# Optimization experiments

Hardware: AMD Instinct MI355X
Metric: run time of the kernel (lower is better)

The kernel has to match this reference:

```python
import jax, jax.numpy as jnp
import numpy as np

B, S, E = 2, 2048, 2048
A, H = 2048, 16  # attention_dim, n_heads
HD = A // H      # head_dim = 128
ROPE_THETA = 10000.0


def setup_inputs() -> dict:
    key = jax.random.key(0)
    k1, k2, k3 = jax.random.split(key, 3)
    x = jax.random.normal(k1, (B, S, E), dtype=jnp.float32)
    W_qkv = jax.random.normal(k2, (E, 3 * A), dtype=jnp.float32) * 0.02
    W_out = jax.random.normal(k3, (A, E), dtype=jnp.float32) * 0.02
    return {"x": x, "W_qkv": W_qkv, "W_out": W_out}


def _apply_rope(x):
    # x: (B, H, S, D); interleaved rotary pairs (rotary-embedding-torch default)
    b, h, s, d = x.shape
    inv_freq = 1.0 / (ROPE_THETA ** (jnp.arange(0, d, 2, dtype=jnp.float32) / d))
    freqs = jnp.arange(s, dtype=jnp.float32)[:, None] * inv_freq[None, :]  # (S, D/2)
    cos, sin = jnp.cos(freqs), jnp.sin(freqs)
    xr = x.reshape(b, h, s, d // 2, 2)
    x1, x2 = xr[..., 0], xr[..., 1]
    o1 = x1 * cos - x2 * sin
    o2 = x1 * sin + x2 * cos
    return jnp.stack([o1, o2], axis=-1).reshape(b, h, s, d)


def reference(x, W_qkv, W_out):
    b, s, _ = x.shape
    qkv = (x @ W_qkv).reshape(b, s, 3, H, HD)          # (B,S,3,H,hd)
    qkv = jnp.moveaxis(qkv, 3, 1)                      # movedim(-2,1) -> (B,H,S,3,hd)
    q, k, v = qkv[..., 0, :], qkv[..., 1, :], qkv[..., 2, :]
    q = _apply_rope(q)
    k = _apply_rope(k)
    scale = 1.0 / jnp.sqrt(jnp.asarray(HD, dtype=x.dtype))
    scores = jnp.einsum("bhqd,bhkd->bhqk", q, k) * scale
    attn = jax.nn.softmax(scores, axis=-1)
    out = jnp.einsum("bhqk,bhkd->bhqd", attn, v)       # (B,H,S,hd)
    out = out.transpose(0, 2, 1, 3).reshape(b, s, A)   # (B,S,A)
    return out @ W_out
```

## Files before the change

kernel.cpp:

```cpp
#include <hip/hip_runtime.h>
#include <math.h>

typedef float  f32x4 __attribute__((ext_vector_type(4)));
typedef short  s16x8 __attribute__((ext_vector_type(8)));
typedef short  s16x4 __attribute__((ext_vector_type(4)));
typedef unsigned short u16;
typedef unsigned int u32;

static __device__ __forceinline__ u16 f32_to_bf16_rne(float f) {
    u32 u = __builtin_bit_cast(u32, f);
    u32 r = u + 0x7fffu + ((u >> 16) & 1u);
    return (u16)(r >> 16);
}
static __device__ __forceinline__ u16 f32_to_bf16_rhu(float f) {
    u32 u = __builtin_bit_cast(u32, f);
    return (u16)((u + 0x8000u) >> 16);
}
static __device__ __forceinline__ float bf16_to_f32(u16 h) {
    return __builtin_bit_cast(float, (u32)h << 16);
}

static __device__ __forceinline__ void gl2lds16(const void* g, void* l) {
    __builtin_amdgcn_global_load_lds(
        (const __attribute__((address_space(1))) u32*)g,
        (__attribute__((address_space(3))) u32*)l, 16, 0, 0);
}

__global__ void k_cast(const float* __restrict__ in, u16* __restrict__ out) {
    int i = (blockIdx.x * 256 + threadIdx.x) * 4;
    float4 v = *reinterpret_cast<const float4*>(in + i);
    ushort4 u;
    u.x = f32_to_bf16_rne(v.x); u.y = f32_to_bf16_rne(v.y);
    u.z = f32_to_bf16_rne(v.z); u.w = f32_to_bf16_rne(v.w);
    *reinterpret_cast<ushort4*>(out + i) = u;
}

__global__ void k_transpose_cast(const float* __restrict__ in, u16* __restrict__ out,
                                 int R, int C) {
    __shared__ __align__(16) float tile[64 * 68];
    const int ct = blockIdx.x, rt = blockIdx.y;
    const int t = threadIdx.x;
    const int tr = t >> 4;
    const int tc4 = (t & 15) * 4;
#pragma unroll
    for (int rn = 0; rn < 4; ++rn) {
        int r = rn * 16 + tr;
        float4 v = *reinterpret_cast<const float4*>(in + (size_t)(rt * 64 + r) * C + ct * 64 + tc4);
        *reinterpret_cast<float4*>(&tile[r * 68 + tc4]) = v;
    }
    __syncthreads();
#pragma unroll
    for (int rn = 0; rn < 4; ++rn) {
        int oc = rn * 16 + tr;
        ushort4 u;
        u.x = f32_to_bf16_rne(tile[(tc4 + 0) * 68 + oc]);
        u.y = f32_to_bf16_rne(tile[(tc4 + 1) * 68 + oc]);
        u.z = f32_to_bf16_rne(tile[(tc4 + 2) * 68 + oc]);
        u.w = f32_to_bf16_rne(tile[(tc4 + 3) * 68 + oc]);
        *reinterpret_cast<ushort4*>(out + (size_t)(ct * 64 + oc) * R + rt * 64 + tc4) = u;
    }
}

template<bool BF16OUT, bool ROPE>
__global__ __launch_bounds__(256) void k_gemm_bt(const u16* __restrict__ Amat,
                                                 const u16* __restrict__ Bt,
                                                 void* __restrict__ Cout,
                                                 int M, int N, int K) {
    __shared__ __align__(16) u16 As[128 * 64];
    __shared__ __align__(16) u16 Bs[128 * 64];
    const int t = threadIdx.x;
    const int lane = t & 63, wave = t >> 6;
    const int m16 = lane & 15, qd = lane >> 4;
    const int wm = (wave >> 1) * 64, wn = (wave & 1) * 64;
    const size_t m0 = (size_t)blockIdx.y * 128, n0 = (size_t)blockIdx.x * 128;
    const int srow = lane >> 3;
    const int schunk = (lane & 7) ^ srow;

    f32x4 acc[4][4] = {};

    for (int k0 = 0; k0 < K; k0 += 64) {
#pragma unroll
        for (int j = 0; j < 4; ++j) {
            int rbase = j * 32 + wave * 8;
            int r = rbase + srow;
            gl2lds16(Amat + (m0 + r) * (size_t)K + k0 + schunk * 8, &As[rbase * 64]);
            gl2lds16(Bt   + (n0 + r) * (size_t)K + k0 + schunk * 8, &Bs[rbase * 64]);
        }
        __syncthreads();
#pragma unroll
        for (int kh = 0; kh < 2; ++kh) {
            s16x8 af[4], bf[4];
#pragma unroll
            for (int i = 0; i < 4; ++i) {
                int ra = wm + i * 16 + m16;
                int pa = (kh * 4 + qd) ^ (ra & 7);
                af[i] = *reinterpret_cast<const s16x8*>(&As[ra * 64 + pa * 8]);
                int rb = wn + i * 16 + m16;
                int pb = (kh * 4 + qd) ^ (rb & 7);
                bf[i] = *reinterpret_cast<const s16x8*>(&Bs[rb * 64 + pb * 8]);
            }
#pragma unroll
            for (int i = 0; i < 4; ++i)
#pragma unroll
                for (int jj = 0; jj < 4; ++jj)
                    acc[i][jj] = __builtin_amdgcn_mfma_f32_16x16x32_bf16(af[i], bf[jj], acc[i][jj], 0, 0, 0);
        }
        __syncthreads();
    }
    if (ROPE && n0 < 4096) {
        float invf[4];
#pragma unroll
        for (int j = 0; j < 4; ++j) {
            int pi = ((int)(wn + j * 16 + m16) & 127) >> 1;
            invf[j] = __expf(-0.14391156831f * (float)pi);
        }
#pragma unroll
        for (int i = 0; i < 4; ++i)
#pragma unroll
            for (int j = 0; j < 4; ++j)
#pragma unroll
                for (int r = 0; r < 4; ++r) {
                    float v = acc[i][j][r];
                    float p = __shfl_xor(v, 1);
                    size_t row = m0 + wm + i * 16 + qd * 4 + r;
                    float f = (float)(int)(row & 2047) * invf[j];
                    float sn, cs;
                    __sincosf(f, &sn, &cs);
                    float res = (m16 & 1) ? fmaf(p, sn, v * cs) : fmaf(v, cs, -p * sn);
                    size_t col = n0 + wn + j * 16 + m16;
                    ((u16*)Cout)[row * N + col] = f32_to_bf16_rne(res);
                }
    } else {
#pragma unroll
        for (int i = 0; i < 4; ++i)
#pragma unroll
            for (int j = 0; j < 4; ++j)
#pragma unroll
                for (int r = 0; r < 4; ++r) {
                    size_t row = m0 + wm + i * 16 + qd * 4 + r;
                    size_t col = n0 + wn + j * 16 + m16;
                    if (BF16OUT)
                        ((u16*)Cout)[row * N + col] = f32_to_bf16_rne(acc[i][j][r]);
                    else
                        ((float*)Cout)[row * N + col] = acc[i][j][r];
                }
    }
}

__global__ void k_transpose_v(const u16* __restrict__ qkv, u16* __restrict__ vt) {
    __shared__ u16 tile[64 * 68];
    const int st = blockIdx.x;
    const int bhd = blockIdx.y;
    const int bh = bhd >> 1, dt = bhd & 1;
    const u16* src = qkv + (size_t)(bh >> 4) * 2048 * 6144 + 4096 + (size_t)(bh & 15) * 128 + dt * 64;
    const int t = threadIdx.x, tr = t >> 4, tc4 = (t & 15) * 4;
#pragma unroll
    for (int rn = 0; rn < 4; ++rn) {
        int s = rn * 16 + tr;
        *reinterpret_cast<ushort4*>(&tile[s * 68 + tc4]) =
            *reinterpret_cast<const ushort4*>(src + (size_t)(st * 64 + s) * 6144 + tc4);
    }
    __syncthreads();
    u16* dst = vt + ((size_t)bh * 128 + dt * 64) * 2048 + st * 64;
#pragma unroll
    for (int rn = 0; rn < 4; ++rn) {
        int d = rn * 16 + tr;
        ushort4 u;
        u.x = tile[(tc4 + 0) * 68 + d];
        u.y = tile[(tc4 + 1) * 68 + d];
        u.z = tile[(tc4 + 2) * 68 + d];
        u.w = tile[(tc4 + 3) * 68 + d];
        *reinterpret_cast<ushort4*>(dst + (size_t)d * 2048 + tc4) = u;
    }
}

__global__ __launch_bounds__(256, 2) void k_flash(const u16* __restrict__ qkv,
                                                  const u16* __restrict__ vt,
                                                  u16* __restrict__ out) {
    __shared__ __align__(16) u16 KS[128 * 136];
    __shared__ __align__(16) u16 VS[128 * 136];
    const int t = threadIdx.x, lane = t & 63, wave = t >> 6;
    const int m16 = lane & 15, qd = lane >> 4;
    const int bh = blockIdx.y, b = bh >> 4, h = bh & 15;
    const int q0 = blockIdx.x * 128;
    const int wq = wave * 32;
    const u16* Qg = qkv + (size_t)b * 2048 * 6144 + (size_t)h * 128;
    const u16* Kg = Qg + 2048;
    const u16* Vtg = vt + (size_t)bh * 128 * 2048;
    const float C2 = 0.12751743f;

    s16x8 qf[2][4];
#pragma unroll
    for (int mi = 0; mi < 2; ++mi)
#pragma unroll
        for (int kc = 0; kc < 4; ++kc)
            qf[mi][kc] = *reinterpret_cast<const s16x8*>(
                Qg + (size_t)(q0 + wq + mi * 16 + m16) * 6144 + kc * 32 + qd * 8);

    f32x4 accO[2][8] = {};
    float mrow[2] = {-1e30f, -1e30f};
    float lrow[2] = {0.f, 0.f};

    const int strow = t >> 4;
    const int stc = (t & 15) * 8;

    for (int kt = 0; kt < 16; ++kt) {
        const int s0 = kt * 128;
        __syncthreads();
#pragma unroll
        for (int rd = 0; rd < 8; ++rd) {
            int row = rd * 16 + strow;
            *reinterpret_cast<s16x8*>(&KS[row * 136 + stc]) =
                *reinterpret_cast<const s16x8*>(Kg + (size_t)(s0 + row) * 6144 + stc);
            *reinterpret_cast<s16x8*>(&VS[row * 136 + stc]) =
                *reinterpret_cast<const s16x8*>(Vtg + (size_t)row * 2048 + s0 + stc);
        }
        __syncthreads();

        f32x4 accS[2][8] = {};
#pragma unroll
        for (int kc = 0; kc < 4; ++kc)
#pragma unroll
            for (int nj = 0; nj < 8; ++nj) {
                s16x8 kf = *reinterpret_cast<const s16x8*>(
                    &KS[(nj * 16 + m16) * 136 + (kc * 4 + qd) * 8]);
                accS[0][nj] = __builtin_amdgcn_mfma_f32_16x16x32_bf16(kf, qf[0][kc], accS[0][nj], 0, 0, 0);
                accS[1][nj] = __builtin_amdgcn_mfma_f32_16x16x32_bf16(kf, qf[1][kc], accS[1][nj], 0, 0, 0);
            }

        s16x4 pk[2][8];
        float aO[2][4];
#pragma unroll
        for (int mi = 0; mi < 2; ++mi) {
            float mx = accS[mi][0][0];
#pragma unroll
            for (int nj = 0; nj < 8; ++nj)
#pragma unroll
                for (int r = 0; r < 4; ++r) mx = fmaxf(mx, accS[mi][nj][r]);
            mx *= C2;
            mx = fmaxf(mx, __shfl_xor(mx, 16));
            mx = fmaxf(mx, __shfl_xor(mx, 32));
            float mn = fmaxf(mrow[mi], mx);
            float alpha = exp2f(mrow[mi] - mn);
            mrow[mi] = mn;
            float ls = 0.f;
#pragma unroll
            for (int nj = 0; nj < 8; ++nj) {
                float p0 = exp2f(accS[mi][nj][0] * C2 - mn);
                float p1 = exp2f(accS[mi][nj][1] * C2 - mn);
                float p2 = exp2f(accS[mi][nj][2] * C2 - mn);
                float p3 = exp2f(accS[mi][nj][3] * C2 - mn);
                ls += (p0 + p1) + (p2 + p3);
                s16x4 pv;
                pv[0] = (short)f32_to_bf16_rhu(p0);
                pv[1] = (short)f32_to_bf16_rhu(p1);
                pv[2] = (short)f32_to_bf16_rhu(p2);
                pv[3] = (short)f32_to_bf16_rhu(p3);
                pk[mi][nj] = pv;
            }
            ls += __shfl_xor(ls, 16);
            ls += __shfl_xor(ls, 32);
            lrow[mi] = lrow[mi] * alpha + ls;
#pragma unroll
            for (int r = 0; r < 4; ++r)
                aO[mi][r] = __shfl(alpha, qd * 4 + r);
#pragma unroll
            for (int dj = 0; dj < 8; ++dj)
#pragma unroll
                for (int r = 0; r < 4; ++r) accO[mi][dj][r] *= aO[mi][r];
        }

#pragma unroll
        for (int kb = 0; kb < 4; ++kb) {
            s16x8 af0 = __builtin_shufflevector(pk[0][2 * kb], pk[0][2 * kb + 1],
                                                0, 1, 2, 3, 4, 5, 6, 7);
            s16x8 af1 = __builtin_shufflevector(pk[1][2 * kb], pk[1][2 * kb + 1],
                                                0, 1, 2, 3, 4, 5, 6, 7);
#pragma unroll
            for (int dj = 0; dj < 8; ++dj) {
                const u16* vrow = &VS[(dj * 16 + m16) * 136 + kb * 32 + qd * 4];
                s16x4 lo = *reinterpret_cast<const s16x4*>(vrow);
                s16x4 hi = *reinterpret_cast<const s16x4*>(vrow + 16);
                s16x8 vf = __builtin_shufflevector(lo, hi, 0, 1, 2, 3, 4, 5, 6, 7);
                accO[0][dj] = __builtin_amdgcn_mfma_f32_16x16x32_bf16(af0, vf, accO[0][dj], 0, 0, 0);
                accO[1][dj] = __builtin_amdgcn_mfma_f32_16x16x32_bf16(af1, vf, accO[1][dj], 0, 0, 0);
            }
        }
    }
#pragma unroll
    for (int mi = 0; mi < 2; ++mi) {
        float invl = 1.0f / lrow[mi];
        float iv[4];
#pragma unroll
        for (int r = 0; r < 4; ++r) iv[r] = __shfl(invl, qd * 4 + r);
#pragma unroll
        for (int r = 0; r < 4; ++r) {
            size_t row = (size_t)b * 2048 + q0 + wq + mi * 16 + qd * 4 + r;
#pragma unroll
            for (int dj = 0; dj < 8; ++dj)
                out[row * 2048 + h * 128 + dj * 16 + m16] =
                    f32_to_bf16_rne(accO[mi][dj][r] * iv[r]);
        }
    }
}

extern "C" void kernel_launch(void* const* d_in, const int* in_sizes, int n_in,
                              void* d_out, int out_size, void* d_ws, size_t ws_size,
                              hipStream_t stream) {
    const float* x     = (const float*)d_in[0];
    const float* W_qkv = (const float*)d_in[1];
    const float* W_out = (const float*)d_in[2];
    float* out = (float*)d_out;

    char* ws = (char*)d_ws;
    u16* xb   = (u16*)(ws);
    u16* Wqt  = (u16*)(ws + (16u << 20));
    u16* Wot  = (u16*)(ws + (40u << 20));
    u16* qkvb = (u16*)(ws + (48u << 20));
    u16* attn = (u16*)(ws + (96u << 20));
    u16* vtg  = (u16*)(ws + (112u << 20));

    k_cast<<<8192, 256, 0, stream>>>(x, xb);
    k_transpose_cast<<<dim3(96, 32), 256, 0, stream>>>(W_qkv, Wqt, 2048, 6144);
    k_transpose_cast<<<dim3(32, 32), 256, 0, stream>>>(W_out, Wot, 2048, 2048);
    k_gemm_bt<true, true><<<dim3(48, 32), 256, 0, stream>>>(xb, Wqt, qkvb, 4096, 6144, 2048);
    k_transpose_v<<<dim3(32, 64), 256, 0, stream>>>(qkvb, vtg);
    k_flash<<<dim3(16, 32), 256, 0, stream>>>(qkvb, vtg, attn);
    k_gemm_bt<false, false><<<dim3(16, 32), 256, 0, stream>>>(attn, Wot, out, 4096, 2048, 2048);
}
```

Baseline: 455.1 us.

## Restructure flash kernel to 8 waves of 16 query rows with register-staged loads

The flash attention block moves from 4 waves handling 32 query rows each to 8 waves handling 16 rows each. This halves per-wave register state so more waves can be resident and hide latency. K/V tile loads are now issued into registers before the barrier and then stored to LDS. V is stored in a permuted column order so each PV fragment is read with a single 16-byte LDS load. The softmax path also switches to the hardware exp2 intrinsic, fused multiply-add and paired bf16 packing. The cost is that each K/V tile in LDS is now shared by fewer query rows per wave, and the larger block adds barrier overhead.

After: 411.7 us. 1.11x faster.

```diff
diff --git a/kernel.cpp b/kernel.cpp
--- a/kernel.cpp
+++ b/kernel.cpp
@@ -12,9 +12,10 @@
     u32 r = u + 0x7fffu + ((u >> 16) & 1u);
     return (u16)(r >> 16);
 }
-static __device__ __forceinline__ u16 f32_to_bf16_rhu(float f) {
-    u32 u = __builtin_bit_cast(u32, f);
-    return (u16)((u + 0x8000u) >> 16);
+static __device__ __forceinline__ u32 pack_bf16_rhu(float a, float b) {
+    u32 ua = __builtin_bit_cast(u32, a);
+    u32 ub = __builtin_bit_cast(u32, b);
+    return ((ua + 0x8000u) >> 16) | ((ub + 0x8000u) & 0xffff0000u);
 }
 static __device__ __forceinline__ float bf16_to_f32(u16 h) {
     return __builtin_bit_cast(float, (u32)h << 16);
@@ -174,7 +175,7 @@
     }
 }
 
-__global__ __launch_bounds__(256, 2) void k_flash(const u16* __restrict__ qkv,
+__global__ __launch_bounds__(512, 4) void k_flash(const u16* __restrict__ qkv,
                                                   const u16* __restrict__ vt,
                                                   u16* __restrict__ out) {
     __shared__ __align__(16) u16 KS[128 * 136];
@@ -183,124 +184,120 @@
     const int m16 = lane & 15, qd = lane >> 4;
     const int bh = blockIdx.y, b = bh >> 4, h = bh & 15;
     const int q0 = blockIdx.x * 128;
-    const int wq = wave * 32;
     const u16* Qg = qkv + (size_t)b * 2048 * 6144 + (size_t)h * 128;
     const u16* Kg = Qg + 2048;
     const u16* Vtg = vt + (size_t)bh * 128 * 2048;
     const float C2 = 0.12751743f;
 
-    s16x8 qf[2][4];
-#pragma unroll
-    for (int mi = 0; mi < 2; ++mi)
-#pragma unroll
-        for (int kc = 0; kc < 4; ++kc)
-            qf[mi][kc] = *reinterpret_cast<const s16x8*>(
-                Qg + (size_t)(q0 + wq + mi * 16 + m16) * 6144 + kc * 32 + qd * 8);
-
-    f32x4 accO[2][8] = {};
-    float mrow[2] = {-1e30f, -1e30f};
-    float lrow[2] = {0.f, 0.f};
-
-    const int strow = t >> 4;
-    const int stc = (t & 15) * 8;
+    int srow[4], scol[4], pi0[4];
+#pragma unroll
+    for (int ci = 0; ci < 4; ++ci) {
+        int idx = ci * 512 + t;
+        int row = idx >> 4, c = idx & 15;
+        srow[ci] = row;
+        scol[ci] = c * 8;
+        pi0[ci] = 32 * (c >> 2) + 16 * (c & 1) + 4 * ((c >> 1) & 1);
+    }
+
+    s16x8 qf[4];
+#pragma unroll
+    for (int kc = 0; kc < 4; ++kc)
+        qf[kc] = *reinterpret_cast<const s16x8*>(
+            Qg + (size_t)(q0 + wave * 16 + m16) * 6144 + kc * 32 + qd * 8);
+
+    f32x4 accO[8] = {};
+    float mrow = -1e30f, lrow = 0.f;
 
     for (int kt = 0; kt < 16; ++kt) {
         const int s0 = kt * 128;
+        s16x8 kreg[4], vreg[4];
+#pragma unroll
+        for (int ci = 0; ci < 4; ++ci) {
+            kreg[ci] = *reinterpret_cast<const s16x8*>(
+                Kg + (size_t)(s0 + srow[ci]) * 6144 + scol[ci]);
+            vreg[ci] = *reinterpret_cast<const s16x8*>(
+                Vtg + (size_t)srow[ci] * 2048 + s0 + scol[ci]);
+        }
         __syncthreads();
 #pragma unroll
-        for (int rd = 0; rd < 8; ++rd) {
-            int row = rd * 16 + strow;
-            *reinterpret_cast<s16x8*>(&KS[row * 136 + stc]) =
-                *reinterpret_cast<const s16x8*>(Kg + (size_t)(s0 + row) * 6144 + stc);
-            *reinterpret_cast<s16x8*>(&VS[row * 136 + stc]) =
-                *reinterpret_cast<const s16x8*>(Vtg + (size_t)row * 2048 + s0 + stc);
+        for (int ci = 0; ci < 4; ++ci) {
+            *reinterpret_cast<s16x8*>(&KS[srow[ci] * 136 + scol[ci]]) = kreg[ci];
+            s16x4 lo = __builtin_shufflevector(vreg[ci], vreg[ci], 0, 1, 2, 3);
+            s16x4 hi = __builtin_shufflevector(vreg[ci], vreg[ci], 4, 5, 6, 7);
+            *reinterpret_cast<s16x4*>(&VS[srow[ci] * 136 + pi0[ci]]) = lo;
+            *reinterpret_cast<s16x4*>(&VS[srow[ci] * 136 + pi0[ci] + 8]) = hi;
         }
         __syncthreads();
 
-        f32x4 accS[2][8] = {};
+        f32x4 accS[8] = {};
 #pragma unroll
         for (int kc = 0; kc < 4; ++kc)
 #pragma unroll
             for (int nj = 0; nj < 8; ++nj) {
                 s16x8 kf = *reinterpret_cast<const s16x8*>(
                     &KS[(nj * 16 + m16) * 136 + (kc * 4 + qd) * 8]);
-                accS[0][nj] = __builtin_amdgcn_mfma_f32_16x16x32_bf16(kf, qf[0][kc], accS[0][nj], 0, 0, 0);
-                accS[1][nj] = __builtin_amdgcn_mfma_f32_16x16x32_bf16(kf, qf[1][kc], accS[1][nj], 0, 0, 0);
+                accS[nj] = __builtin_amdgcn_mfma_f32_16x16x32_bf16(kf, qf[kc], accS[nj], 0, 0, 0);
             }
 
-        s16x4 pk[2][8];
-        float aO[2][4];
-#pragma unroll
-        for (int mi = 0; mi < 2; ++mi) {
-            float mx = accS[mi][0][0];
-#pragma unroll
-            for (int nj = 0; nj < 8; ++nj)
-#pragma unroll
-                for (int r = 0; r < 4; ++r) mx = fmaxf(mx, accS[mi][nj][r]);
-            mx *= C2;
-            mx = fmaxf(mx, __shfl_xor(mx, 16));
-            mx = fmaxf(mx, __shfl_xor(mx, 32));
-            float mn = fmaxf(mrow[mi], mx);
-            float alpha = exp2f(mrow[mi] - mn);
-            mrow[mi] = mn;
-            float ls = 0.f;
-#pragma unroll
-            for (int nj = 0; nj < 8; ++nj) {
-                float p0 = exp2f(accS[mi][nj][0] * C2 - mn);
-                float p1 = exp2f(accS[mi][nj][1] * C2 - mn);
-                float p2 = exp2f(accS[mi][nj][2] * C2 - mn);
-                float p3 = exp2f(accS[mi][nj][3] * C2 - mn);
-                ls += (p0 + p1) + (p2 + p3);
-                s16x4 pv;
-                pv[0] = (short)f32_to_bf16_rhu(p0);
-                pv[1] = (short)f32_to_bf16_rhu(p1);
-                pv[2] = (short)f32_to_bf16_rhu(p2);
-                pv[3] = (short)f32_to_bf16_rhu(p3);
-                pk[mi][nj] = pv;
+        float mx = accS[0][0];
+#pragma unroll
+        for (int nj = 0; nj < 8; ++nj)
+#pragma unroll
+            for (int r = 0; r < 4; ++r) mx = fmaxf(mx, accS[nj][r]);
+        mx *= C2;
+        mx = fmaxf(mx, __shfl_xor(mx, 16));
+        mx = fmaxf(mx, __shfl_xor(mx, 32));
+        float mn = fmaxf(mrow, mx);
+        float alpha = __builtin_amdgcn_exp2f(mrow - mn);
+        mrow = mn;
+        float ls = 0.f;
+        s16x4 pk[8];
+#pragma unroll
+        for (int nj = 0; nj < 8; ++nj) {
+            float p0 = __builtin_amdgcn_exp2f(fmaf(accS[nj][0], C2, -mn));
+            float p1 = __builtin_amdgcn_exp2f(fmaf(accS[nj][1], C2, -mn));
+            float p2 = __builtin_amdgcn_exp2f(fmaf(accS[nj][2], C2, -mn));
+            float p3 = __builtin_amdgcn_exp2f(fmaf(accS[nj][3], C2, -mn));
+            ls += (p0 + p1) + (p2 + p3);
+            u32 lo = pack_bf16_rhu(p0, p1);
+            u32 hi = pack_bf16_rhu(p2, p3);
+            uint2 pr = make_uint2(lo, hi);
+            pk[nj] = __builtin_bit_cast(s16x4, pr);
+        }
+        ls += __shfl_xor(ls, 16);
+        ls += __shfl_xor(ls, 32);
+        lrow = lrow * alpha + ls;
+        float aO[4];
+#pragma unroll
+        for (int r = 0; r < 4; ++r) aO[r] = __shfl(alpha, qd * 4 + r);
+#pragma unroll
+        for (int dj = 0; dj < 8; ++dj)
+#pragma unroll
+            for (int r = 0; r < 4; ++r) accO[dj][r] *= aO[r];
+
+#pragma unroll
+        for (int kb = 0; kb < 4; ++kb) {
+            s16x8 af = __builtin_shufflevector(pk[2 * kb], pk[2 * kb + 1],
+                                               0, 1, 2, 3, 4, 5, 6, 7);
+#pragma unroll
+            for (int dj = 0; dj < 8; ++dj) {
+                s16x8 vf = *reinterpret_cast<const s16x8*>(
+                    &VS[(dj * 16 + m16) * 136 + kb * 32 + qd * 8]);
+                accO[dj] = __builtin_amdgcn_mfma_f32_16x16x32_bf16(af, vf, accO[dj], 0, 0, 0);
             }
-            ls += __shfl_xor(ls, 16);
-            ls += __shfl_xor(ls, 32);
-            lrow[mi] = lrow[mi] * alpha + ls;
-#pragma unroll
-            for (int r = 0; r < 4; ++r)
-                aO[mi][r] = __shfl(alpha, qd * 4 + r);
-#pragma unroll
-            for (int dj = 0; dj < 8; ++dj)
-#pragma unroll
-                for (int r = 0; r < 4; ++r) accO[mi][dj][r] *= aO[mi][r];
-        }
-
-#pragma unroll
-        for (int kb = 0; kb < 4; ++kb) {
-            s16x8 af0 = __builtin_shufflevector(pk[0][2 * kb], pk[0][2 * kb + 1],
-                                                0, 1, 2, 3, 4, 5, 6, 7);
-            s16x8 af1 = __builtin_shufflevector(pk[1][2 * kb], pk[1][2 * kb + 1],
-                                                0, 1, 2, 3, 4, 5, 6, 7);
-#pragma unroll
-            for (int dj = 0; dj < 8; ++dj) {
-                const u16* vrow = &VS[(dj * 16 + m16) * 136 + kb * 32 + qd * 4];
-                s16x4 lo = *reinterpret_cast<const s16x4*>(vrow);
-                s16x4 hi = *reinterpret_cast<const s16x4*>(vrow + 16);
-                s16x8 vf = __builtin_shufflevector(lo, hi, 0, 1, 2, 3, 4, 5, 6, 7);
-                accO[0][dj] = __builtin_amdgcn_mfma_f32_16x16x32_bf16(af0, vf, accO[0][dj], 0, 0, 0);
-                accO[1][dj] = __builtin_amdgcn_mfma_f32_16x16x32_bf16(af1, vf, accO[1][dj], 0, 0, 0);
-            }
-        }
-    }
-#pragma unroll
-    for (int mi = 0; mi < 2; ++mi) {
-        float invl = 1.0f / lrow[mi];
-        float iv[4];
-#pragma unroll
-        for (int r = 0; r < 4; ++r) iv[r] = __shfl(invl, qd * 4 + r);
-#pragma unroll
-        for (int r = 0; r < 4; ++r) {
-            size_t row = (size_t)b * 2048 + q0 + wq + mi * 16 + qd * 4 + r;
-#pragma unroll
-            for (int dj = 0; dj < 8; ++dj)
-                out[row * 2048 + h * 128 + dj * 16 + m16] =
-                    f32_to_bf16_rne(accO[mi][dj][r] * iv[r]);
-        }
+        }
+    }
+    float invl = 1.0f / lrow;
+    float iv[4];
+#pragma unroll
+    for (int r = 0; r < 4; ++r) iv[r] = __shfl(invl, qd * 4 + r);
+#pragma unroll
+    for (int r = 0; r < 4; ++r) {
+        size_t row = (size_t)b * 2048 + q0 + wave * 16 + qd * 4 + r;
+#pragma unroll
+        for (int dj = 0; dj < 8; ++dj)
+            out[row * 2048 + h * 128 + dj * 16 + m16] =
+                f32_to_bf16_rne(accO[dj][r] * iv[r]);
     }
 }
 
@@ -325,6 +322,6 @@
     k_transpose_cast<<<dim3(32, 32), 256, 0, stream>>>(W_out, Wot, 2048, 2048);
     k_gemm_bt<true, true><<<dim3(48, 32), 256, 0, stream>>>(xb, Wqt, qkvb, 4096, 6144, 2048);
     k_transpose_v<<<dim3(32, 64), 256, 0, stream>>>(qkvb, vtg);
-    k_flash<<<dim3(16, 32), 256, 0, stream>>>(qkvb, vtg, attn);
+    k_flash<<<dim3(16, 32), 512, 0, stream>>>(qkvb, vtg, attn);
     k_gemm_bt<false, false><<<dim3(16, 32), 256, 0, stream>>>(attn, Wot, out, 4096, 2048, 2048);
 }
```
